# Optimization experiments

Measured on AMD Instinct MI355X. Metric: run time of the kernel, lower is better.

Reference implementation:

```python
import jax, jax.numpy as jnp
import numpy as np

WIN = 7


def rel_index(win: int) -> jnp.ndarray:
    ys, xs = jnp.meshgrid(jnp.arange(win), jnp.arange(win), indexing='ij')
    coords = jnp.stack([ys.reshape(-1), xs.reshape(-1)], axis=-1)  # (S, 2)
    diff = coords[None, :, :] - coords[:, None, :] + (win - 1)     # (S, S, 2)
    return diff[..., 0] * (2 * win - 1) + diff[..., 1]             # (S, S)


def setup_inputs() -> dict:
    key = jax.random.key(0)
    ks = jax.random.split(key, 5)
    B, WN, S, C, H = 64, 64, WIN * WIN, 192, 6
    X = jax.random.normal(ks[0], (B, WN, S, C), dtype=jnp.float32)
    # torch nn.Linear(emb_dim, 3*emb_dim) -> store as (in, out) for x @ W
    Wqkv = jax.random.normal(ks[1], (C, 3 * C), dtype=jnp.float32) * 0.02
    bqkv = jnp.zeros((3 * C,), dtype=jnp.float32)
    Wo = jax.random.normal(ks[2], (C, C), dtype=jnp.float32) * 0.02
    bo = jnp.zeros((C,), dtype=jnp.float32)
    bias_table = jax.random.normal(ks[3], ((2 * WIN - 1) ** 2, H), dtype=jnp.float32) * 0.02
    return {"X": X, "Wqkv": Wqkv, "bqkv": bqkv, "Wo": Wo, "bo": bo, "bias_table": bias_table}


def reference(X, Wqkv, bqkv, Wo, bo, bias_table):
    B, WN, S, C = X.shape
    H = bias_table.shape[1]
    D = C // H
    scale = D ** -0.5
    # qkv projection: (B, WN, S, 3C) -> (3, B, WN, H, S, D)
    qkv = (X @ Wqkv + bqkv).reshape(B, WN, S, 3, H, D).transpose(3, 0, 1, 4, 2, 5)
    q, k, v = qkv[0], qkv[1], qkv[2]
    attn = jnp.einsum('bwhqd,bwhkd->bwhqk', q, k) * scale  # (B, WN, H, S, S)
    # gathered relative position bias: (S, S, H) -> (H, S, S)
    idx = rel_index(WIN)
    bias = bias_table[idx].transpose(2, 0, 1)
    attn = attn + bias[None, None]
    proba = jax.nn.softmax(attn, axis=-1)  # dropout omitted (eval mode)
    out = jnp.einsum('bwhqk,bwhkd->bwhqd', proba, v)  # (B, WN, H, S, D)
    out = out.transpose(0, 1, 3, 2, 4).reshape(B, WN, S, C)
    return out @ Wo + bo
```

## Files before the change

kernel.cpp:

```cpp
#include <hip/hip_runtime.h>
#include <hip/hip_bf16.h>


typedef __attribute__((ext_vector_type(4))) float f32x4;
typedef __attribute__((ext_vector_type(8))) short bf16x8;
typedef __attribute__((ext_vector_type(4))) unsigned short u16x4;

#define SCALE 0.17677669529663689f
#define MFMA(a, b, acc) __builtin_amdgcn_mfma_f32_16x16x32_bf16(a, b, acc, 0, 0, 0)

__device__ __forceinline__ unsigned short f2bf(float f) {
  union { float f; unsigned int u; } v; v.f = f;
  return (unsigned short)((v.u + 0x7FFFu + ((v.u >> 16) & 1u)) >> 16);
}

__device__ __forceinline__ void gll16(const unsigned short* src, unsigned short* dst) {
  __builtin_amdgcn_global_load_lds(
      (const __attribute__((address_space(1))) unsigned int*)src,
      (__attribute__((address_space(3))) unsigned int*)dst, 16, 0, 0);
}

__global__ void wprep(const float* __restrict__ Wqkv, const float* __restrict__ Wo,
                      unsigned short* __restrict__ WqkvTs, unsigned short* __restrict__ WoTs) {
  int i = blockIdx.x * 256 + threadIdx.x;
  if (i < 576 * 192) {
    int n = i / 192, k = i % 192;
    int ch = n >> 6, row = n & 63;
    int dst = ch * 12288 + row * 192 + (((k >> 3) ^ (row & 7)) << 3) + (k & 7);
    WqkvTs[dst] = f2bf(Wqkv[k * 576 + n]);
  }
  if (i < 192 * 192) {
    int n = i / 192, k = i % 192;
    int dst = n * 192 + (((k >> 3) ^ (n & 7)) << 3) + (k & 7);
    WoTs[dst] = f2bf(Wo[k * 192 + n]);
  }
}

__global__ __launch_bounds__(512, 4)
void qkv_gemm(const float* __restrict__ X, const unsigned short* __restrict__ WqkvTs,
              const float* __restrict__ bqkv, unsigned short* __restrict__ qkv) {
  __shared__ __align__(16) unsigned short Bs[2][12288];
  __shared__ __align__(16) unsigned short scr[8][1152];
  __shared__ float biasLds[576];

  const int tid = threadIdx.x, w8 = tid >> 6, lane = tid & 63;
  const int g = lane >> 4, c = lane & 15;
  const int mt = w8 & 3, half = w8 >> 2;
  const size_t bm = (size_t)blockIdx.x * 128;
  const size_t r0 = bm + mt * 32;
  const f32x4 z = {0.f, 0.f, 0.f, 0.f};

  #pragma unroll
  for (int jj = 0; jj < 3; ++jj)
    gll16(WqkvTs + (w8 * 3 + jj) * 512 + lane * 8, &Bs[0][(w8 * 3 + jj) * 512]);
  for (int j = tid; j < 576; j += 512) biasLds[j] = bqkv[j];

  bf16x8 af0[6], af1[6];
  #pragma unroll
  for (int m = 0; m < 2; ++m) {
    const float* xr = X + (r0 + m * 16 + c) * 192;
    #pragma unroll
    for (int ks = 0; ks < 6; ++ks) {
      f32x4 lo = *(const f32x4*)(xr + ks * 32 + g * 8);
      f32x4 hi = *(const f32x4*)(xr + ks * 32 + g * 8 + 4);
      bf16x8 a;
      a[0] = (short)f2bf(lo[0]); a[1] = (short)f2bf(lo[1]);
      a[2] = (short)f2bf(lo[2]); a[3] = (short)f2bf(lo[3]);
      a[4] = (short)f2bf(hi[0]); a[5] = (short)f2bf(hi[1]);
      a[6] = (short)f2bf(hi[2]); a[7] = (short)f2bf(hi[3]);
      if (m) af1[ks] = a; else af0[ks] = a;
    }
  }
  asm volatile("s_waitcnt vmcnt(0)\n\ts_barrier" ::: "memory");
  __builtin_amdgcn_sched_barrier(0);

  unsigned short* sw = scr[w8];
  for (int nc = 0; nc < 9; ++nc) {
    const int cur = nc & 1;
    if (nc < 8) {
      #pragma unroll
      for (int jj = 0; jj < 3; ++jj)
        gll16(WqkvTs + (nc + 1) * 12288 + (w8 * 3 + jj) * 512 + lane * 8,
              &Bs[cur ^ 1][(w8 * 3 + jj) * 512]);
    }
    f32x4 acc0[2] = {z, z}, acc1[2] = {z, z};
    #pragma unroll
    for (int ks = 0; ks < 6; ++ks) {
      #pragma unroll
      for (int nf = 0; nf < 2; ++nf) {
        const bf16x8 bv = *(const bf16x8*)(
            &Bs[cur][(half * 32 + nf * 16 + c) * 192 + (((ks * 4 + g) ^ (c & 7)) << 3)]);
        acc0[nf] = MFMA(af0[ks], bv, acc0[nf]);
        acc1[nf] = MFMA(af1[ks], bv, acc1[nf]);
      }
    }
    #pragma unroll
    for (int m = 0; m < 2; ++m) {
      #pragma unroll
      for (int nf = 0; nf < 2; ++nf) {
        const float bb = biasLds[nc * 64 + half * 32 + nf * 16 + c];
        const f32x4 a = m ? acc1[nf] : acc0[nf];
        #pragma unroll
        for (int r = 0; r < 4; ++r)
          sw[(4 * g + r) * 72 + nf * 16 + c] = f2bf(a[r] + bb);
      }
      const uint4 o = *(const uint4*)(sw + c * 72 + g * 8);
      *(uint4*)(qkv + (r0 + m * 16 + c) * 576 + nc * 64 + half * 32 + g * 8) = o;
    }

    if (nc < 8) {
      asm volatile("s_waitcnt vmcnt(2)\n\ts_barrier" ::: "memory");
      __builtin_amdgcn_sched_barrier(0);
    }
  }
}

__global__ __launch_bounds__(512, 4)
void attn_win(unsigned short* __restrict__ qkv, const float* __restrict__ btab) {
  __shared__ __align__(16) unsigned short Ks[64 * 200];
  __shared__ __align__(16) unsigned short Vt[192 * 72];
  __shared__ __align__(16) unsigned short scr[8][1152];
  __shared__ float biasF[1014];

  const int tid = threadIdx.x, w8 = tid >> 6, lane = tid & 63;
  const int g = lane >> 4, c = lane & 15;
  const int mt = w8 & 3, hw = w8 >> 2;
  const size_t tokbase = (size_t)blockIdx.x * 49;
  const f32x4 z = {0.f, 0.f, 0.f, 0.f};

  for (int j = tid; j < 1014; j += 512) biasF[j] = btab[j];
  for (int j = tid; j < 360; j += 512) {
    uint4 zz = {0, 0, 0, 0};
    *(uint4*)(&Ks[(49 + j / 24) * 200 + (j % 24) * 8]) = zz;
  }
  for (int j = tid; j < 2880; j += 512) Vt[(j / 15) * 72 + 49 + j % 15] = 0;
  for (int j = tid; j < 1176; j += 512) {
    int row = j / 24, ch = j % 24;
    *(uint4*)(&Ks[row * 200 + ch * 8]) =
        *(const uint4*)(qkv + (tokbase + row) * 576 + 192 + ch * 8);
  }
  for (int j = tid; j < 1176; j += 512) {
    int row = j / 24, ch = j % 24;
    uint4 v = *(const uint4*)(qkv + (tokbase + row) * 576 + 384 + ch * 8);
    const unsigned short* e = (const unsigned short*)&v;
    #pragma unroll
    for (int m = 0; m < 8; ++m) {
      int k = (ch + m) & 7;
      Vt[(ch * 8 + k) * 72 + row] = e[k];
    }
  }

  const int qbase = mt * 16;
  const int q = qbase + c;
  const bool qvalid = q < 49;
  const int qc = qvalid ? q : 48;

  bf16x8 bqh[3];
  #pragma unroll
  for (int hi = 0; hi < 3; ++hi)
    bqh[hi] = *(const bf16x8*)(qkv + (tokbase + qc) * 576 + (hw * 3 + hi) * 32 + g * 8);

  __syncthreads();

  const int qoff6 = ((6 - qc / 7) * 13 + (6 - qc % 7)) * 6;
  int kb6[16];
  #pragma unroll
  for (int i = 0; i < 16; ++i) {
    int k = (i >> 2) * 16 + g * 4 + (i & 3);
    int kk = k < 49 ? k : 48;
    kb6[i] = ((kk / 7) * 13 + (kk % 7)) * 6;
  }
  unsigned short* Pw = scr[w8];

  #pragma unroll
  for (int hi = 0; hi < 3; ++hi) {
    const int h = hw * 3 + hi;
    const bf16x8 bq = bqh[hi];
    const int cofs = h * 32 + g * 8;
    f32x4 s0 = MFMA(*(const bf16x8*)(Ks + (c) * 200 + cofs), bq, z);
    f32x4 s1 = MFMA(*(const bf16x8*)(Ks + (16 + c) * 200 + cofs), bq, z);
    f32x4 s2 = MFMA(*(const bf16x8*)(Ks + (32 + c) * 200 + cofs), bq, z);
    f32x4 s3 = MFMA(*(const bf16x8*)(Ks + (48 + c) * 200 + cofs), bq, z);

    float p[16];
    float mx = -3e38f;
    #pragma unroll
    for (int i = 0; i < 16; ++i) {
      const int t = i >> 2, r = i & 3;
      const int k = t * 16 + g * 4 + r;
      const float sv = (t == 0) ? s0[r] : (t == 1) ? s1[r] : (t == 2) ? s2[r] : s3[r];
      const float b = biasF[kb6[i] + qoff6 + h];
      const float lg = (qvalid && (k < 49)) ? fmaf(sv, SCALE, b) : -1e30f;
      p[i] = lg;
      mx = fmaxf(mx, lg);
    }
    mx = fmaxf(mx, __shfl_xor(mx, 16));
    mx = fmaxf(mx, __shfl_xor(mx, 32));
    float sum = 0.f;
    #pragma unroll
    for (int i = 0; i < 16; ++i) { p[i] = __expf(p[i] - mx); sum += p[i]; }
    sum += __shfl_xor(sum, 16);
    sum += __shfl_xor(sum, 32);
    const float inv = 1.0f / sum;
    #pragma unroll
    for (int t = 0; t < 4; ++t) {
      u16x4 pkv;
      #pragma unroll
      for (int r = 0; r < 4; ++r) pkv[r] = f2bf(p[t * 4 + r] * inv);
      *(u16x4*)(Pw + c * 72 + t * 16 + g * 4) = pkv;
    }

    f32x4 o0 = z, o1 = z;
    #pragma unroll
    for (int ks = 0; ks < 2; ++ks) {
      const bf16x8 ap = *(const bf16x8*)(Pw + c * 72 + ks * 32 + g * 8);
      const bf16x8 v0 = *(const bf16x8*)(Vt + (h * 32 + c) * 72 + ks * 32 + g * 8);
      const bf16x8 v1 = *(const bf16x8*)(Vt + (h * 32 + 16 + c) * 72 + ks * 32 + g * 8);
      o0 = MFMA(ap, v0, o0);
      o1 = MFMA(ap, v1, o1);
    }
    #pragma unroll
    for (int r = 0; r < 4; ++r) {
      Pw[(4 * g + r) * 72 + c]      = f2bf(o0[r]);
      Pw[(4 * g + r) * 72 + 16 + c] = f2bf(o1[r]);
    }
    uint4 ov = *(const uint4*)(Pw + c * 72 + g * 8);
    if (qvalid)
      *(uint4*)(qkv + (tokbase + q) * 576 + h * 32 + g * 8) = ov;
  }
}

__global__ __launch_bounds__(512, 4)
void out_gemm(const unsigned short* __restrict__ qkv, const unsigned short* __restrict__ WoTs,
              const float* __restrict__ bo, float* __restrict__ out) {
  __shared__ __align__(16) unsigned short Ws[192 * 192];

  const int tid = threadIdx.x, w8 = tid >> 6, lane = tid & 63;
  const int g = lane >> 4, c = lane & 15;
  const int mt = w8 & 3, half = w8 >> 2;
  const size_t bm = (size_t)blockIdx.x * 128;
  const size_t r0 = bm + mt * 32;
  const f32x4 z = {0.f, 0.f, 0.f, 0.f};

  #pragma unroll
  for (int jj = 0; jj < 9; ++jj)
    gll16(WoTs + (w8 * 9 + jj) * 512 + lane * 8, &Ws[(w8 * 9 + jj) * 512]);

  bf16x8 af0[6], af1[6];
  #pragma unroll
  for (int ks = 0; ks < 6; ++ks) {
    af0[ks] = *(const bf16x8*)(qkv + (r0 + c) * 576 + ks * 32 + g * 8);
    af1[ks] = *(const bf16x8*)(qkv + (r0 + 16 + c) * 576 + ks * 32 + g * 8);
  }
  __syncthreads();

  #pragma unroll
  for (int nf = 0; nf < 6; ++nf) {
    const int col = half * 96 + nf * 16 + c;
    f32x4 acc0 = z, acc1 = z;
    #pragma unroll
    for (int ks = 0; ks < 6; ++ks) {
      const bf16x8 bv = *(const bf16x8*)(
          &Ws[col * 192 + (((ks * 4 + g) ^ (c & 7)) << 3)]);
      acc0 = MFMA(af0[ks], bv, acc0);
      acc1 = MFMA(af1[ks], bv, acc1);
    }
    const float bb = bo[col];
    #pragma unroll
    for (int r = 0; r < 4; ++r) {
      out[(r0 + 4 * g + r) * 192 + col]      = acc0[r] + bb;
      out[(r0 + 16 + 4 * g + r) * 192 + col] = acc1[r] + bb;
    }
  }
}

extern "C" void kernel_launch(void* const* d_in, const int* in_sizes, int n_in,
                              void* d_out, int out_size, void* d_ws, size_t ws_size,
                              hipStream_t stream) {
  (void)in_sizes; (void)n_in; (void)out_size; (void)ws_size;
  const float* X    = (const float*)d_in[0];
  const float* Wqkv = (const float*)d_in[1];
  const float* bqkv = (const float*)d_in[2];
  const float* Wo   = (const float*)d_in[3];
  const float* bo   = (const float*)d_in[4];
  const float* btab = (const float*)d_in[5];

  unsigned short* WqkvTs = (unsigned short*)d_ws;
  unsigned short* WoTs   = WqkvTs + 576 * 192;
  unsigned short* qkv    = WoTs + 192 * 192;

  wprep<<<432, 256, 0, stream>>>(Wqkv, Wo, WqkvTs, WoTs);
  qkv_gemm<<<1568, 512, 0, stream>>>(X, WqkvTs, bqkv, qkv);
  attn_win<<<4096, 512, 0, stream>>>(qkv, btab);
  out_gemm<<<1568, 512, 0, stream>>>(qkv, WoTs, bo, (float*)d_out);
}
```

Measured before the change: 298.3 us.

## Split QKV GEMM into three column panels and swap MFMA operands for vector stores

The QKV projection now launches three times as many blocks, each loading one 192x192 weight panel into LDS once, instead of streaming nine double-buffered chunks with per-chunk barriers. Swapping the MFMA operand order transposes the accumulator layout, so each lane holds four consecutive output columns. That lets the bias load and the bf16 or f32 stores be written as direct vector accesses without the LDS scratch transpose, in both the QKV and output GEMMs. The cost is that each X tile is read and converted to bf16 three times, and each block must load its whole weight panel before computing.

After: 375.0 us. 1.26x slower.

```diff
diff --git a/kernel.cpp b/kernel.cpp
--- a/kernel.cpp
+++ b/kernel.cpp
@@ -39,21 +39,19 @@
 __global__ __launch_bounds__(512, 4)
 void qkv_gemm(const float* __restrict__ X, const unsigned short* __restrict__ WqkvTs,
               const float* __restrict__ bqkv, unsigned short* __restrict__ qkv) {
-  __shared__ __align__(16) unsigned short Bs[2][12288];
-  __shared__ __align__(16) unsigned short scr[8][1152];
-  __shared__ float biasLds[576];
+  __shared__ __align__(16) unsigned short Ws[192 * 192];
 
   const int tid = threadIdx.x, w8 = tid >> 6, lane = tid & 63;
   const int g = lane >> 4, c = lane & 15;
   const int mt = w8 & 3, half = w8 >> 2;
-  const size_t bm = (size_t)blockIdx.x * 128;
-  const size_t r0 = bm + mt * 32;
+  const int panel = blockIdx.x % 3;
+  const size_t r0 = (size_t)(blockIdx.x / 3) * 128 + mt * 32;
   const f32x4 z = {0.f, 0.f, 0.f, 0.f};
 
-  #pragma unroll
-  for (int jj = 0; jj < 3; ++jj)
-    gll16(WqkvTs + (w8 * 3 + jj) * 512 + lane * 8, &Bs[0][(w8 * 3 + jj) * 512]);
-  for (int j = tid; j < 576; j += 512) biasLds[j] = bqkv[j];
+  const unsigned short* wp = WqkvTs + panel * 36864;
+  #pragma unroll
+  for (int jj = 0; jj < 9; ++jj)
+    gll16(wp + (w8 * 9 + jj) * 512 + lane * 8, &Ws[(w8 * 9 + jj) * 512]);
 
   bf16x8 af0[6], af1[6];
   #pragma unroll
@@ -71,47 +69,25 @@
       if (m) af1[ks] = a; else af0[ks] = a;
     }
   }
-  asm volatile("s_waitcnt vmcnt(0)\n\ts_barrier" ::: "memory");
-  __builtin_amdgcn_sched_barrier(0);
-
-  unsigned short* sw = scr[w8];
-  for (int nc = 0; nc < 9; ++nc) {
-    const int cur = nc & 1;
-    if (nc < 8) {
-      #pragma unroll
-      for (int jj = 0; jj < 3; ++jj)
-        gll16(WqkvTs + (nc + 1) * 12288 + (w8 * 3 + jj) * 512 + lane * 8,
-              &Bs[cur ^ 1][(w8 * 3 + jj) * 512]);
-    }
-    f32x4 acc0[2] = {z, z}, acc1[2] = {z, z};
+  __syncthreads();
+
+  #pragma unroll
+  for (int nf = 0; nf < 6; ++nf) {
+    const int ocl = half * 96 + nf * 16;
+    f32x4 acc0 = z, acc1 = z;
     #pragma unroll
     for (int ks = 0; ks < 6; ++ks) {
-      #pragma unroll
-      for (int nf = 0; nf < 2; ++nf) {
-        const bf16x8 bv = *(const bf16x8*)(
-            &Bs[cur][(half * 32 + nf * 16 + c) * 192 + (((ks * 4 + g) ^ (c & 7)) << 3)]);
-        acc0[nf] = MFMA(af0[ks], bv, acc0[nf]);
-        acc1[nf] = MFMA(af1[ks], bv, acc1[nf]);
-      }
-    }
-    #pragma unroll
-    for (int m = 0; m < 2; ++m) {
-      #pragma unroll
-      for (int nf = 0; nf < 2; ++nf) {
-        const float bb = biasLds[nc * 64 + half * 32 + nf * 16 + c];
-        const f32x4 a = m ? acc1[nf] : acc0[nf];
-        #pragma unroll
-        for (int r = 0; r < 4; ++r)
-          sw[(4 * g + r) * 72 + nf * 16 + c] = f2bf(a[r] + bb);
-      }
-      const uint4 o = *(const uint4*)(sw + c * 72 + g * 8);
-      *(uint4*)(qkv + (r0 + m * 16 + c) * 576 + nc * 64 + half * 32 + g * 8) = o;
-    }
-
-    if (nc < 8) {
-      asm volatile("s_waitcnt vmcnt(2)\n\ts_barrier" ::: "memory");
-      __builtin_amdgcn_sched_barrier(0);
-    }
+      const bf16x8 bv = *(const bf16x8*)(
+          &Ws[(ocl + c) * 192 + (((ks * 4 + g) ^ (c & 7)) << 3)]);
+      acc0 = MFMA(bv, af0[ks], acc0);
+      acc1 = MFMA(bv, af1[ks], acc1);
+    }
+    const f32x4 bb = *(const f32x4*)(bqkv + panel * 192 + ocl + 4 * g);
+    u16x4 s0, s1;
+    #pragma unroll
+    for (int r = 0; r < 4; ++r) { s0[r] = f2bf(acc0[r] + bb[r]); s1[r] = f2bf(acc1[r] + bb[r]); }
+    *(u16x4*)(qkv + (r0 + c) * 576      + panel * 192 + ocl + 4 * g) = s0;
+    *(u16x4*)(qkv + (r0 + 16 + c) * 576 + panel * 192 + ocl + 4 * g) = s1;
   }
 }
 
@@ -238,8 +214,7 @@
   const int tid = threadIdx.x, w8 = tid >> 6, lane = tid & 63;
   const int g = lane >> 4, c = lane & 15;
   const int mt = w8 & 3, half = w8 >> 2;
-  const size_t bm = (size_t)blockIdx.x * 128;
-  const size_t r0 = bm + mt * 32;
+  const size_t r0 = (size_t)blockIdx.x * 128 + mt * 32;
   const f32x4 z = {0.f, 0.f, 0.f, 0.f};
 
   #pragma unroll
@@ -256,21 +231,18 @@
 
   #pragma unroll
   for (int nf = 0; nf < 6; ++nf) {
-    const int col = half * 96 + nf * 16 + c;
+    const int ocl = half * 96 + nf * 16;
     f32x4 acc0 = z, acc1 = z;
     #pragma unroll
     for (int ks = 0; ks < 6; ++ks) {
       const bf16x8 bv = *(const bf16x8*)(
-          &Ws[col * 192 + (((ks * 4 + g) ^ (c & 7)) << 3)]);
-      acc0 = MFMA(af0[ks], bv, acc0);
-      acc1 = MFMA(af1[ks], bv, acc1);
-    }
-    const float bb = bo[col];
-    #pragma unroll
-    for (int r = 0; r < 4; ++r) {
-      out[(r0 + 4 * g + r) * 192 + col]      = acc0[r] + bb;
-      out[(r0 + 16 + 4 * g + r) * 192 + col] = acc1[r] + bb;
-    }
+          &Ws[(ocl + c) * 192 + (((ks * 4 + g) ^ (c & 7)) << 3)]);
+      acc0 = MFMA(bv, af0[ks], acc0);
+      acc1 = MFMA(bv, af1[ks], acc1);
+    }
+    const f32x4 bb = *(const f32x4*)(bo + ocl + 4 * g);
+    *(f32x4*)(out + (r0 + c) * 192 + ocl + 4 * g)      = acc0 + bb;
+    *(f32x4*)(out + (r0 + 16 + c) * 192 + ocl + 4 * g) = acc1 + bb;
   }
 }
 
@@ -290,7 +262,7 @@
   unsigned short* qkv    = WoTs + 192 * 192;
 
   wprep<<<432, 256, 0, stream>>>(Wqkv, Wo, WqkvTs, WoTs);
-  qkv_gemm<<<1568, 512, 0, stream>>>(X, WqkvTs, bqkv, qkv);
+  qkv_gemm<<<4704, 512, 0, stream>>>(X, WqkvTs, bqkv, qkv);
   attn_win<<<4096, 512, 0, stream>>>(qkv, btab);
   out_gemm<<<1568, 512, 0, stream>>>(qkv, WoTs, bo, (float*)d_out);
 }
```
